# Optimization experiments

Measured on AMD Instinct MI355X. Metric: run time of the kernel, lower is better.

Reference implementation:

```python
import jax, jax.numpy as jnp
import numpy as np

# Model dims (match init_kwargs / Mamba2 defaults)
B, T = 2, 4096
D_MODEL = 1024
D_STATE = 128
D_CONV = 4
EXPAND = 2
D_INNER = EXPAND * D_MODEL          # 2048
HEADDIM = 64                        # Mamba2 default
NHEADS = D_INNER // HEADDIM         # 32
D_IN_PROJ = 2 * D_INNER + 2 * D_STATE + NHEADS  # z, xBC, dt
CONV_DIM = D_INNER + 2 * D_STATE    # conv over x, B, C


def setup_inputs() -> dict:
    key = jax.random.key(0)
    ks = jax.random.split(key, 8)
    return {
        "x": jax.random.normal(ks[0], (B, D_MODEL, T), jnp.float32),
        "ln_w": jnp.ones((D_MODEL,), jnp.float32),
        "ln_b": jnp.zeros((D_MODEL,), jnp.float32),
        "W_in": jax.random.normal(ks[1], (D_IN_PROJ, D_MODEL), jnp.float32) * 0.02,
        "conv_w": jax.random.normal(ks[2], (CONV_DIM, D_CONV), jnp.float32) * 0.2,
        "conv_b": jnp.zeros((CONV_DIM,), jnp.float32),
        "dt_bias": jax.random.normal(ks[3], (NHEADS,), jnp.float32) * 0.5,
        "A_log": jnp.log(0.5 + jax.random.uniform(ks[4], (NHEADS,)) * 4.0),
        "D": jnp.ones((NHEADS,), jnp.float32),
        "rms_w": jnp.ones((D_INNER,), jnp.float32),
        "W_out": jax.random.normal(ks[5], (D_MODEL, D_INNER), jnp.float32) * 0.02,
        "hidden_state": jnp.zeros((B, NHEADS, HEADDIM, D_STATE), jnp.float32),
    }


def _silu(v):
    return v * jax.nn.sigmoid(v)


def _forward(x, ln_w, ln_b, W_in, conv_w, conv_b, dt_bias, A_log, Dp, rms_w, W_out, h0):
    # x: [B, d_model, T] -> [B, T, d_model]
    xt = x.transpose(0, 2, 1)
    # LayerNorm
    mu = xt.mean(-1, keepdims=True)
    var = ((xt - mu) ** 2).mean(-1, keepdims=True)
    xn = (xt - mu) * jax.lax.rsqrt(var + 1e-5) * ln_w + ln_b
    # in_proj -> z, xBC, dt
    zxbcdt = xn @ W_in.T                       # [B, T, D_IN_PROJ]
    z = zxbcdt[..., :D_INNER]
    xBC = zxbcdt[..., D_INNER:D_INNER + CONV_DIM]
    dt = zxbcdt[..., D_INNER + CONV_DIM:]      # [B, T, H]
    # causal depthwise conv over time (kernel D_CONV), then SiLU
    xpad = jnp.pad(xBC, ((0, 0), (D_CONV - 1, 0), (0, 0)))
    conv = sum(conv_w[:, k] * xpad[:, k:k + T, :] for k in range(D_CONV)) + conv_b
    xBC = _silu(conv)
    xin = xBC[..., :D_INNER].reshape(B, T, NHEADS, HEADDIM)
    Bm = xBC[..., D_INNER:D_INNER + D_STATE]   # [B, T, N]
    Cm = xBC[..., D_INNER + D_STATE:]          # [B, T, N]
    # selective SSM parameters
    dt = jax.nn.softplus(dt + dt_bias)         # [B, T, H]
    A = -jnp.exp(A_log)                        # [H]
    dA = jnp.exp(dt * A)                       # [B, T, H]
    xdt = xin * dt[..., None]                  # [B, T, H, P]

    def step(h, inp):
        dA_t, x_t, B_t, C_t = inp              # [B,H], [B,H,P], [B,N], [B,N]
        h = h * dA_t[:, :, None, None] + x_t[..., None] * B_t[:, None, None, :]
        y_t = jnp.einsum("bhpn,bn->bhp", h, C_t)
        return h, y_t

    hT, ys = jax.lax.scan(
        step, h0,
        (dA.transpose(1, 0, 2), xdt.transpose(1, 0, 2, 3),
         Bm.transpose(1, 0, 2), Cm.transpose(1, 0, 2)))
    y = ys.transpose(1, 0, 2, 3) + Dp[None, None, :, None] * xin  # [B,T,H,P]
    y = y.reshape(B, T, D_INNER)
    # gated RMSNorm then out_proj
    g = y * _silu(z)
    g = g * jax.lax.rsqrt((g * g).mean(-1, keepdims=True) + 1e-5) * rms_w
    out = (g @ W_out.T).transpose(0, 2, 1)     # back to [B, d_model, T]
    return out, hT


def reference(x, ln_w, ln_b, W_in, conv_w, conv_b, dt_bias, A_log, D, rms_w, W_out, hidden_state):
    return _forward(x, ln_w, ln_b, W_in, conv_w, conv_b, dt_bias, A_log, D, rms_w, W_out, hidden_state)
```

## Files before the change

kernel.cpp:

```cpp
#include <hip/hip_runtime.h>
#include <hip/hip_bf16.h>
#include <math.h>

#define BB 2
#define TT 4096
#define DM 1024
#define DSTATE 128
#define DI 2048
#define HD 64
#define NH 32
#define DIP 4384
#define CD 2304

#define NC 8
#define CL 512
#define FL 64
#define FPC (CL / FL)
#define SELEMS ((size_t)BB * NH * HD * DSTATE)

#define NP1 4480
#define KSPLIT 16

typedef __attribute__((ext_vector_type(8))) short bf16x8;
typedef __attribute__((ext_vector_type(4))) float f32x4;

__device__ inline void gload16(const void* g, void* l) {
    __builtin_amdgcn_global_load_lds(
        (const __attribute__((address_space(1))) void*)g,
        (__attribute__((address_space(3))) void*)l, 16, 0, 0);
}

__device__ inline short f2bs(float f) {
    __hip_bfloat16 h = __float2bfloat16(f);
    union { __hip_bfloat16 h; short s; } u;
    u.h = h;
    return u.s;
}
__device__ inline float b2f(short s) {
    union { float f; unsigned u; } u;
    u.u = ((unsigned)(unsigned short)s) << 16;
    return u.f;
}

__global__ __launch_bounds__(256) void ln_stats_kernel(const float* __restrict__ x,
                                                       float* __restrict__ mu,
                                                       float* __restrict__ rs) {
    __shared__ float sred[2][8][32];
    int tid = threadIdx.x;
    int tl = tid & 31;
    int ds = tid >> 5;
    int t = (blockIdx.x & 127) * 32 + tl;
    int b = blockIdx.x >> 7;
    const float* xb = x + (size_t)b * DM * TT + (size_t)ds * 128 * TT + t;
    float s = 0.f, ss = 0.f;
#pragma unroll 8
    for (int d = 0; d < 128; d++) {
        float v = xb[(size_t)d * TT];
        s += v;
        ss += v * v;
    }
    sred[0][ds][tl] = s;
    sred[1][ds][tl] = ss;
    __syncthreads();
    if (tid < 32) {
        float st = 0.f, sst = 0.f;
#pragma unroll
        for (int q = 0; q < 8; q++) { st += sred[0][q][tid]; sst += sred[1][q][tid]; }
        float m = st * (1.f / DM);
        float var = sst * (1.f / DM) - m * m;
        int idx = b * TT + (blockIdx.x & 127) * 32 + tid;
        mu[idx] = m;
        rs[idx] = rsqrtf(var + 1e-5f);
    }
}

__global__ __launch_bounds__(256) void xn_kernel(const float* __restrict__ x,
                                                 const float* __restrict__ mu,
                                                 const float* __restrict__ rs,
                                                 const float* __restrict__ ln_w,
                                                 const float* __restrict__ ln_b,
                                                 __hip_bfloat16* __restrict__ xn) {
    __shared__ float tile[64][65];
    int tid = threadIdx.x;
    int t0 = blockIdx.x * 64, d0 = blockIdx.y * 64, b = blockIdx.z;
#pragma unroll
    for (int i = 0; i < 64; i += 4) {
        int dl = i + (tid >> 6);
        tile[dl][tid & 63] = x[(size_t)b * DM * TT + (size_t)(d0 + dl) * TT + t0 + (tid & 63)];
    }
    __syncthreads();
#pragma unroll
    for (int i = 0; i < 64; i += 8) {
        int tl = i + (tid >> 5);
        int kk = (tid & 31) * 2;
        int m = b * TT + t0 + tl;
        float mu_m = mu[m], rs_m = rs[m];
        float v0 = (tile[kk][tl] - mu_m) * rs_m * ln_w[d0 + kk] + ln_b[d0 + kk];
        float v1 = (tile[kk + 1][tl] - mu_m) * rs_m * ln_w[d0 + kk + 1] + ln_b[d0 + kk + 1];
        __hip_bfloat162 pk;
        pk.x = __float2bfloat16(v0);
        pk.y = __float2bfloat16(v1);
        *(__hip_bfloat162*)(xn + (size_t)m * DM + d0 + kk) = pk;
    }
}

__global__ __launch_bounds__(256) void cvt_pad_kernel(const float* __restrict__ src,
                                                      __hip_bfloat16* __restrict__ dst,
                                                      int src_n, int tot_n) {
    int i = (blockIdx.x * 256 + threadIdx.x) * 4;
    if (i >= tot_n) return;
    float4 v = (i < src_n) ? *(const float4*)(src + i) : make_float4(0.f, 0.f, 0.f, 0.f);
    __hip_bfloat162 p0, p1;
    p0.x = __float2bfloat16(v.x); p0.y = __float2bfloat16(v.y);
    p1.x = __float2bfloat16(v.z); p1.y = __float2bfloat16(v.w);
    *(__hip_bfloat162*)(dst + i) = p0;
    *(__hip_bfloat162*)(dst + i + 2) = p1;
}

__global__ __launch_bounds__(256) void gemm1_mfma(const __hip_bfloat16* __restrict__ Wb,
                                                  const __hip_bfloat16* __restrict__ xn,
                                                  short* __restrict__ zx) {
    __shared__ short As[128][64];
    __shared__ short Bs[128][64];
    int tid = threadIdx.x;
    int lane = tid & 63;
    int wave = tid >> 6;
    int wr = wave >> 1, wc = wave & 1;
    int id = blockIdx.x;
    int xcd = id & 7;
    int pos = id >> 3;
    int j0 = (pos >> 3) * 128;
    int m0 = (xcd * 8 + (pos & 7)) * 128;
    int srow = tid >> 3;
    int skc = (((tid & 7) ^ ((tid >> 3) & 7)) * 8);

    f32x4 acc[4][4] = {};

    for (int k0 = 0; k0 < DM; k0 += 64) {
        __syncthreads();
#pragma unroll
        for (int q = 0; q < 4; q++) {
            gload16(Wb + (size_t)(j0 + q * 32 + srow) * DM + k0 + skc,
                    ((short*)As) + q * 2048 + wave * 512);
            gload16(xn + (size_t)(m0 + q * 32 + srow) * DM + k0 + skc,
                    ((short*)Bs) + q * 2048 + wave * 512);
        }
        asm volatile("s_waitcnt vmcnt(0)" ::: "memory");
        __syncthreads();
#pragma unroll
        for (int ks = 0; ks < 2; ks++) {
            int pch = (((ks * 4) + (lane >> 4)) ^ (lane & 7)) * 8;
            bf16x8 af[4], bfr[4];
#pragma unroll
            for (int i = 0; i < 4; i++)
                af[i] = *(const bf16x8*)&As[wr * 64 + i * 16 + (lane & 15)][pch];
#pragma unroll
            for (int n = 0; n < 4; n++)
                bfr[n] = *(const bf16x8*)&Bs[wc * 64 + n * 16 + (lane & 15)][pch];
#pragma unroll
            for (int i = 0; i < 4; i++)
#pragma unroll
                for (int n = 0; n < 4; n++)
                    acc[i][n] = __builtin_amdgcn_mfma_f32_16x16x32_bf16(af[i], bfr[n], acc[i][n], 0, 0, 0);
        }
    }
#pragma unroll
    for (int i = 0; i < 4; i++) {
        int j = j0 + wr * 64 + i * 16 + ((lane >> 4) << 2);
        if (j < DIP) {
#pragma unroll
            for (int n = 0; n < 4; n++) {
                int m = m0 + wc * 64 + n * 16 + (lane & 15);
                short4 s4;
                s4.x = f2bs(acc[i][n][0]); s4.y = f2bs(acc[i][n][1]);
                s4.z = f2bs(acc[i][n][2]); s4.w = f2bs(acc[i][n][3]);
                *(short4*)(zx + (size_t)m * DIP + j) = s4;
            }
        }
    }
}

__global__ __launch_bounds__(256) void gemm1_strip(const float* __restrict__ x,
                                                   const float* __restrict__ mu,
                                                   const float* __restrict__ rs,
                                                   const float* __restrict__ ln_w,
                                                   const float* __restrict__ ln_b,
                                                   const float* __restrict__ Win,
                                                   float* __restrict__ partial) {
    __shared__ float As[16][64];
    __shared__ float Ws[64][17];
    int tid = threadIdx.x;
    int tx = tid & 15;
    int ty = tid >> 4;
    int j0 = 4352;
    int kq = blockIdx.x;
    int m0 = blockIdx.y * 64;
    int b = m0 >> 12;
    int t0 = m0 & 4095;
    const float* Xb = x + (size_t)b * DM * TT + t0;

    int lr = tid >> 4;
    int lc = (tid & 15) * 4;
    int wr = tid >> 2;
    int wc = (tid & 3) * 4;

    float acc[4][4] = {};
    int kbeg = kq * (DM / KSPLIT);
    for (int k0 = kbeg; k0 < kbeg + DM / KSPLIT; k0 += 16) {
        float4 xv = *(const float4*)(Xb + (size_t)(k0 + lr) * TT + lc);
        float4 muv = *(const float4*)(&mu[m0 + lc]);
        float4 rsv = *(const float4*)(&rs[m0 + lc]);
        float lw = ln_w[k0 + lr], lb = ln_b[k0 + lr];
        As[lr][lc]     = (xv.x - muv.x) * rsv.x * lw + lb;
        As[lr][lc + 1] = (xv.y - muv.y) * rsv.y * lw + lb;
        As[lr][lc + 2] = (xv.z - muv.z) * rsv.z * lw + lb;
        As[lr][lc + 3] = (xv.w - muv.w) * rsv.w * lw + lb;

        int j = j0 + wr;
        float4 wv = make_float4(0.f, 0.f, 0.f, 0.f);
        if (j < DIP) wv = *(const float4*)(Win + (size_t)j * DM + k0 + wc);
        Ws[wr][wc] = wv.x; Ws[wr][wc + 1] = wv.y; Ws[wr][wc + 2] = wv.z; Ws[wr][wc + 3] = wv.w;
        __syncthreads();
#pragma unroll
        for (int kk = 0; kk < 16; kk++) {
            float4 a4 = *(const float4*)&As[kk][ty * 4];
            float a[4] = {a4.x, a4.y, a4.z, a4.w};
            float bv[4];
#pragma unroll
            for (int n = 0; n < 4; n++) bv[n] = Ws[tx * 4 + n][kk];
#pragma unroll
            for (int i = 0; i < 4; i++)
#pragma unroll
                for (int n = 0; n < 4; n++)
                    acc[i][n] = fmaf(a[i], bv[n], acc[i][n]);
        }
        __syncthreads();
    }
#pragma unroll
    for (int i = 0; i < 4; i++) {
        int m = m0 + ty * 4 + i;
        int hh = tx * 4;
        if (hh < NH) {
            float4 v = make_float4(acc[i][0], acc[i][1], acc[i][2], acc[i][3]);
            *(float4*)(partial + ((size_t)kq * BB * TT + m) * NH + hh) = v;
        }
    }
}

__global__ __launch_bounds__(256) void dt_reduce_kernel(const float* __restrict__ partial,
                                                        const float* __restrict__ dt_bias,
                                                        float* __restrict__ dtv) {
    int i = blockIdx.x * 256 + threadIdx.x;
    int hh = i & (NH - 1);
    float s = 0.f;
#pragma unroll
    for (int kq = 0; kq < KSPLIT; kq++)
        s += partial[(size_t)kq * BB * TT * NH + i];
    float raw = s + dt_bias[hh];
    dtv[i] = (raw > 20.f) ? raw : log1pf(expf(raw));
}

__global__ __launch_bounds__(256) void conv_kernel(const short* __restrict__ zx,
                                                   const float* __restrict__ cw,
                                                   const float* __restrict__ cb,
                                                   short* __restrict__ xBC) {
    int gid = blockIdx.x * 256 + threadIdx.x;
    int cq = gid % (CD / 8);
    int tq = (gid / (CD / 8)) % (TT / 4);
    int b  = gid / ((CD / 8) * (TT / 4));
    int c = cq * 8, tb = tq * 4;
    const short* src = zx + (size_t)b * TT * DIP + DI + c;

    float wv[8][4];
    float acc[4][8];
#pragma unroll
    for (int e = 0; e < 8; e++) {
        float4 w4 = *(const float4*)(cw + (c + e) * 4);
        wv[e][0] = w4.x; wv[e][1] = w4.y; wv[e][2] = w4.z; wv[e][3] = w4.w;
        float bias = cb[c + e];
#pragma unroll
        for (int o = 0; o < 4; o++) acc[o][e] = bias;
    }

#pragma unroll
    for (int r = 0; r < 7; r++) {
        int ts = tb - 3 + r;
        if (ts >= 0) {
            bf16x8 v = *(const bf16x8*)(src + (size_t)ts * DIP);
            float rowf[8];
#pragma unroll
            for (int e = 0; e < 8; e++) rowf[e] = b2f(v[e]);
#pragma unroll
            for (int o = 0; o < 4; o++) {
                if (o <= r && r <= o + 3) {
                    int k = r - o;
#pragma unroll
                    for (int e = 0; e < 8; e++)
                        acc[o][e] = fmaf(wv[e][k], rowf[e], acc[o][e]);
                }
            }
        }
    }
#pragma unroll
    for (int o = 0; o < 4; o++) {
        short out[8];
#pragma unroll
        for (int e = 0; e < 8; e++) {
            float sg = 1.f / (1.f + expf(-acc[o][e]));
            out[e] = f2bs(acc[o][e] * sg);
        }
        *(bf16x8*)(xBC + ((size_t)b * TT + tb + o) * CD + c) = *(bf16x8*)out;
    }
}

__global__ __launch_bounds__(256, 2) void scan_reduce_ssd(const short* __restrict__ xBC,
                                                          const float* __restrict__ dtg,
                                                          const float* __restrict__ A_log,
                                                          float* __restrict__ S,
                                                          float* __restrict__ P) {
    int tid = threadIdx.x;
    int wave = tid >> 6, lane = tid & 63;
    int l4 = lane >> 4, l16 = lane & 15;
    int c = blockIdx.x, hh = blockIdx.y, b = blockIdx.z;
    int cbase = c * CL;

    __shared__ __align__(16) short BtL[64][136];
    __shared__ __align__(16) short XdL[64][72];
    __shared__ __align__(16) float sdt[64];
    __shared__ __align__(16) float sL[64];
    __shared__ __align__(16) float sW[64];

    f32x4 acc_h[2][4];
#pragma unroll
    for (int i = 0; i < 2; i++)
#pragma unroll
        for (int pq = 0; pq < 4; pq++) acc_h[i][pq] = (f32x4){0.f, 0.f, 0.f, 0.f};
    float Lsum = 0.f;

    float expA = expf(A_log[hh]);
    const float* dtb = dtg + (size_t)b * TT * NH + hh;
    const short* xb = xBC + (size_t)b * TT * CD;

#pragma unroll 1
    for (int f = 0; f < FPC; f++) {
        int t0 = cbase + f * FL;
        if (tid < 64) {
            float val = dtb[(size_t)(t0 + tid) * NH];
            sdt[tid] = val;
            float v = -expA * val;
#pragma unroll
            for (int off = 1; off < 64; off <<= 1) {
                float u = __shfl_up(v, off);
                if (lane >= off) v += u;
            }
            sL[tid] = v;
            float lt = __shfl(v, 63);
            sW[tid] = expf(lt - v);
        }
        {
            int r = tid >> 2, q = tid & 3;
            const short* bs = xb + (size_t)(t0 + r) * CD + DI + q * 32;
#pragma unroll
            for (int j = 0; j < 4; j++)
                *(bf16x8*)&BtL[r][q * 32 + j * 8] = *(const bf16x8*)(bs + j * 8);
        }
        __syncthreads();
        {
            int s = tid & 63, pg2 = tid >> 6;
            const short* xs = xb + (size_t)(t0 + s) * CD + hh * HD + pg2 * 16;
            float dw = sdt[s] * sW[s];
            bf16x8 v0 = *(const bf16x8*)xs;
            bf16x8 v1 = *(const bf16x8*)(xs + 8);
#pragma unroll
            for (int j = 0; j < 8; j++) XdL[pg2 * 16 + j][s] = f2bs(b2f(v0[j]) * dw);
#pragma unroll
            for (int j = 0; j < 8; j++) XdL[pg2 * 16 + 8 + j][s] = f2bs(b2f(v1[j]) * dw);
        }
        __syncthreads();
        float Lft = sL[63];
        float Pf = expf(Lft);
        Lsum += Lft;
#pragma unroll
        for (int i = 0; i < 2; i++)
#pragma unroll
            for (int pq = 0; pq < 4; pq++) acc_h[i][pq] *= Pf;
#pragma unroll
        for (int ks = 0; ks < 2; ks++) {
            bf16x8 af2[2], bfw[4];
#pragma unroll
            for (int i = 0; i < 2; i++) {
                int nrow = wave * 32 + i * 16 + l16;
                short e[8];
#pragma unroll
                for (int j = 0; j < 8; j++)
                    e[j] = BtL[ks * 32 + l4 * 8 + j][nrow];
                af2[i] = *(bf16x8*)e;
            }
#pragma unroll
            for (int pq = 0; pq < 4; pq++)
                bfw[pq] = *(const bf16x8*)&XdL[pq * 16 + l16][ks * 32 + l4 * 8];
#pragma unroll
            for (int i = 0; i < 2; i++)
#pragma unroll
                for (int pq = 0; pq < 4; pq++)
                    acc_h[i][pq] = __builtin_amdgcn_mfma_f32_16x16x32_bf16(af2[i], bfw[pq], acc_h[i][pq], 0, 0, 0);
        }
        __syncthreads();
    }

    float* Sp = S + (size_t)c * SELEMS + ((size_t)(b * NH + hh) * HD) * DSTATE;
#pragma unroll
    for (int i = 0; i < 2; i++)
#pragma unroll
        for (int pq = 0; pq < 4; pq++) {
            int nb = wave * 32 + i * 16 + (l4 << 2);
            int p = pq * 16 + l16;
            *(f32x4*)(Sp + (size_t)p * DSTATE + nb) = acc_h[i][pq];
        }
    if (tid == 0) P[(c * BB + b) * NH + hh] = expf(Lsum);
}

__global__ __launch_bounds__(256) void scan_combine_kernel(const float* __restrict__ h0,
                                                           const float* __restrict__ P,
                                                           float* __restrict__ S,
                                                           float* __restrict__ hT) {
    size_t tid = (size_t)blockIdx.x * 256 + threadIdx.x;
    int hh = (int)((tid >> 13) & 31);
    int b = (int)(tid >> 18);
    float h = h0[tid];
#pragma unroll
    for (int c = 0; c < NC; c++) {
        float s = S[(size_t)c * SELEMS + tid];
        S[(size_t)c * SELEMS + tid] = h;
        h = fmaf(P[(c * BB + b) * NH + hh], h, s);
    }
    hT[tid] = h;
}

__global__ __launch_bounds__(256, 2) void scan_emit_ssd(const short* __restrict__ xBC,
                                                        const float* __restrict__ dtg,
                                                        const float* __restrict__ A_log,
                                                        const float* __restrict__ S,
                                                        const float* __restrict__ Dp,
                                                        short* __restrict__ ybq) {
    int tid = threadIdx.x;
    int wave = tid >> 6, lane = tid & 63;
    int l4 = lane >> 4, l16 = lane & 15;
    int c = blockIdx.x, hh = blockIdx.y, b = blockIdx.z;
    int cbase = c * CL;

    __shared__ __align__(16) short CtL[64][136];
    __shared__ __align__(16) short BtL[64][136];
    __shared__ __align__(16) short hL[64][132];
    __shared__ __align__(16) short XdL[64][72];
    __shared__ __align__(16) short XdwL[64][72];
    __shared__ __align__(16) short ML[64][72];
    __shared__ __align__(16) float sdt[64];
    __shared__ __align__(16) float sL[64];
    __shared__ __align__(16) float sW[64];
    __shared__ __align__(16) float sRdt[64];

    f32x4 acc_h[2][4];
    {
        const float* Sp = S + (size_t)c * SELEMS + ((size_t)(b * NH + hh) * HD) * DSTATE;
#pragma unroll
        for (int i = 0; i < 2; i++)
#pragma unroll
            for (int pq = 0; pq < 4; pq++) {
                int nb = wave * 32 + i * 16 + (l4 << 2);
                int p = pq * 16 + l16;
                acc_h[i][pq] = *(const f32x4*)(Sp + (size_t)p * DSTATE + nb);
            }
    }

    float expA = expf(A_log[hh]);
    float Dh = Dp[hh];
    const float* dtb = dtg + (size_t)b * TT * NH + hh;
    const short* xb = xBC + (size_t)b * TT * CD;
    short* yb = ybq + (size_t)b * TT * DI + hh * HD;

    int tg = wave >> 1;
    int sg = wave & 1;

#pragma unroll 1
    for (int f = 0; f < FPC; f++) {
        int t0 = cbase + f * FL;

        if (tid < 64) {
            float val = dtb[(size_t)(t0 + tid) * NH];
            sdt[tid] = val;
            float v = -expA * val;
#pragma unroll
            for (int off = 1; off < 64; off <<= 1) {
                float u = __shfl_up(v, off);
                if (lane >= off) v += u;
            }
            sL[tid] = v;
            float lt = __shfl(v, 63);
            sW[tid] = expf(lt - v);
            sRdt[tid] = 1.f / val;
        }
        {
            int r = tid >> 2, q = tid & 3;
            const short* cs = xb + (size_t)(t0 + r) * CD + DI + DSTATE + q * 32;
            const short* bs = xb + (size_t)(t0 + r) * CD + DI + q * 32;
#pragma unroll
            for (int j = 0; j < 4; j++) {
                *(bf16x8*)&CtL[r][q * 32 + j * 8] = *(const bf16x8*)(cs + j * 8);
                *(bf16x8*)&BtL[r][q * 32 + j * 8] = *(const bf16x8*)(bs + j * 8);
            }
        }
#pragma unroll
        for (int i = 0; i < 2; i++)
#pragma unroll
            for (int pq = 0; pq < 4; pq++) {
                int nb = wave * 32 + i * 16 + (l4 << 2);
                int p = pq * 16 + l16;
                *(short2*)&hL[p][nb] = make_short2(f2bs(acc_h[i][pq][0]), f2bs(acc_h[i][pq][1]));
                *(short2*)&hL[p][nb + 2] = make_short2(f2bs(acc_h[i][pq][2]), f2bs(acc_h[i][pq][3]));
            }
        __syncthreads();

        {
            int s = tid & 63, pg = tid >> 6;
            const short* xs = xb + (size_t)(t0 + s) * CD + hh * HD + pg * 16;
            float dts = sdt[s];
            float dw = dts * sW[s];
            bf16x8 v0 = *(const bf16x8*)xs;
            bf16x8 v1 = *(const bf16x8*)(xs + 8);
#pragma unroll
            for (int j = 0; j < 8; j++) {
                float xv = b2f(v0[j]);
                XdL[pg * 16 + j][s] = f2bs(xv * dts);
                XdwL[pg * 16 + j][s] = f2bs(xv * dw);
            }
#pragma unroll
            for (int j = 0; j < 8; j++) {
                float xv = b2f(v1[j]);
                XdL[pg * 16 + 8 + j][s] = f2bs(xv * dts);
                XdwL[pg * 16 + 8 + j][s] = f2bs(xv * dw);
            }
        }
        __syncthreads();

        {
            f32x4 g[2][2] = {};
#pragma unroll
            for (int ks = 0; ks < 4; ks++) {
                bf16x8 af[2], bfm[2];
#pragma unroll
                for (int i = 0; i < 2; i++)
                    af[i] = *(const bf16x8*)&CtL[tg * 32 + i * 16 + l16][ks * 32 + l4 * 8];
#pragma unroll
                for (int n = 0; n < 2; n++)
                    bfm[n] = *(const bf16x8*)&BtL[sg * 32 + n * 16 + l16][ks * 32 + l4 * 8];
#pragma unroll
                for (int i = 0; i < 2; i++)
#pragma unroll
                    for (int n = 0; n < 2; n++)
                        g[i][n] = __builtin_amdgcn_mfma_f32_16x16x32_bf16(af[i], bfm[n], g[i][n], 0, 0, 0);
            }
#pragma unroll
            for (int i = 0; i < 2; i++) {
                int tb2 = tg * 32 + i * 16 + (l4 << 2);
                float4 Lt = *(const float4*)&sL[tb2];
                float Ltr[4] = {Lt.x, Lt.y, Lt.z, Lt.w};
#pragma unroll
                for (int n = 0; n < 2; n++) {
                    int sE = sg * 32 + n * 16 + l16;
                    float Ls = sL[sE];
#pragma unroll
                    for (int r2 = 0; r2 < 4; r2++) {
                        float m = (sE <= tb2 + r2) ? g[i][n][r2] * expf(Ltr[r2] - Ls) : 0.f;
                        ML[tb2 + r2][sE] = f2bs(m);
                    }
                }
            }
        }
        __syncthreads();

        {
            f32x4 ay[2][2] = {};
            f32x4 ai[2][2] = {};
#pragma unroll
            for (int ks = 0; ks < 2; ks++) {
                bf16x8 af[2], bfp[2];
#pragma unroll
                for (int i = 0; i < 2; i++)
                    af[i] = *(const bf16x8*)&ML[tg * 32 + i * 16 + l16][ks * 32 + l4 * 8];
#pragma unroll
                for (int n = 0; n < 2; n++)
                    bfp[n] = *(const bf16x8*)&XdL[sg * 32 + n * 16 + l16][ks * 32 + l4 * 8];
#pragma unroll
                for (int i = 0; i < 2; i++)
#pragma unroll
                    for (int n = 0; n < 2; n++)
                        ay[i][n] = __builtin_amdgcn_mfma_f32_16x16x32_bf16(af[i], bfp[n], ay[i][n], 0, 0, 0);
            }
#pragma unroll
            for (int ks = 0; ks < 4; ks++) {
                bf16x8 af[2], bfh[2];
#pragma unroll
                for (int i = 0; i < 2; i++)
                    af[i] = *(const bf16x8*)&CtL[tg * 32 + i * 16 + l16][ks * 32 + l4 * 8];
#pragma unroll
                for (int n = 0; n < 2; n++) {
                    int prow = sg * 32 + n * 16 + l16;
                    int kb = ks * 32 + l4 * 8;
                    union { bf16x8 v; uint2 u2[2]; } hu;
                    hu.u2[0] = *(const uint2*)&hL[prow][kb];
                    hu.u2[1] = *(const uint2*)&hL[prow][kb + 4];
                    bfh[n] = hu.v;
                }
#pragma unroll
                for (int i = 0; i < 2; i++)
#pragma unroll
                    for (int n = 0; n < 2; n++)
                        ai[i][n] = __builtin_amdgcn_mfma_f32_16x16x32_bf16(af[i], bfh[n], ai[i][n], 0, 0, 0);
            }
            float Lft = sL[63];
#pragma unroll
            for (int i = 0; i < 2; i++) {
                int tb2 = tg * 32 + i * 16 + (l4 << 2);
                float4 Lt = *(const float4*)&sL[tb2];
                float4 Rt = *(const float4*)&sRdt[tb2];
                float Ltr[4] = {Lt.x, Lt.y, Lt.z, Lt.w};
                float Rtr[4] = {Rt.x, Rt.y, Rt.z, Rt.w};
#pragma unroll
                for (int n = 0; n < 2; n++) {
                    int p = sg * 32 + n * 16 + l16;
#pragma unroll
                    for (int r2 = 0; r2 < 4; r2++) {
                        float xv = b2f(XdL[p][tb2 + r2]) * Rtr[r2];
                        float yv = ay[i][n][r2] + expf(Ltr[r2]) * ai[i][n][r2] + Dh * xv;
                        yb[(size_t)(t0 + tb2 + r2) * DI + p] = f2bs(yv);
                    }
                }
            }
            float Pf = expf(Lft);
#pragma unroll
            for (int i = 0; i < 2; i++)
#pragma unroll
                for (int pq = 0; pq < 4; pq++)
                    acc_h[i][pq] *= Pf;
#pragma unroll
            for (int ks = 0; ks < 2; ks++) {
                bf16x8 af2[2], bfw[4];
#pragma unroll
                for (int i = 0; i < 2; i++) {
                    int nrow = wave * 32 + i * 16 + l16;
                    short e[8];
#pragma unroll
                    for (int j = 0; j < 8; j++)
                        e[j] = BtL[ks * 32 + l4 * 8 + j][nrow];
                    af2[i] = *(bf16x8*)e;
                }
#pragma unroll
                for (int pq = 0; pq < 4; pq++)
                    bfw[pq] = *(const bf16x8*)&XdwL[pq * 16 + l16][ks * 32 + l4 * 8];
#pragma unroll
                for (int i = 0; i < 2; i++)
#pragma unroll
                    for (int pq = 0; pq < 4; pq++)
                        acc_h[i][pq] = __builtin_amdgcn_mfma_f32_16x16x32_bf16(af2[i], bfw[pq], acc_h[i][pq], 0, 0, 0);
            }
        }
        __syncthreads();
    }
}

__global__ __launch_bounds__(256) void gate_rms_kernel(const short* __restrict__ ybq,
                                                       const short* __restrict__ zx,
                                                       const float* __restrict__ rw,
                                                       __hip_bfloat16* __restrict__ gq) {
    int m = blockIdx.x;
    int tid = threadIdx.x;
    const short* yr = ybq + (size_t)m * DI;
    const short* zr = zx + (size_t)m * DIP;
    int base = tid * 8;
    float gv[8];
    float ss = 0.f;
    bf16x8 yv8 = *(const bf16x8*)(yr + base);
    bf16x8 zv8 = *(const bf16x8*)(zr + base);
#pragma unroll
    for (int i = 0; i < 8; i++) {
        float y = b2f(yv8[i]);
        float z = b2f(zv8[i]);
        float sg = 1.f / (1.f + expf(-z));
        float gg = y * z * sg;
        gv[i] = gg;
        ss += gg * gg;
    }
#pragma unroll
    for (int off = 1; off < 64; off <<= 1) ss += __shfl_xor(ss, off);
    __shared__ float red[4];
    int w = tid >> 6;
    if ((tid & 63) == 0) red[w] = ss;
    __syncthreads();
    float tot = red[0] + red[1] + red[2] + red[3];
    float r = rsqrtf(tot * (1.f / DI) + 1e-5f);
#pragma unroll
    for (int i = 0; i < 8; i += 2) {
        __hip_bfloat162 p;
        p.x = __float2bfloat16(gv[i] * r * rw[base + i]);
        p.y = __float2bfloat16(gv[i + 1] * r * rw[base + i + 1]);
        *(__hip_bfloat162*)(gq + (size_t)m * DI + base + i) = p;
    }
}

__global__ __launch_bounds__(256) void gemm2_mfma(const __hip_bfloat16* __restrict__ gq,
                                                  const __hip_bfloat16* __restrict__ Wob,
                                                  float* __restrict__ out) {
    __shared__ short As[128][64];
    __shared__ short Bs[128][64];
    int tid = threadIdx.x;
    int lane = tid & 63;
    int wave = tid >> 6;
    int wr = wave >> 1, wc = wave & 1;
    int id = blockIdx.x;
    int xcd = id & 7;
    int pos = id >> 3;
    int j0 = (pos >> 3) * 128;
    int m0 = (xcd * 8 + (pos & 7)) * 128;
    int srow = tid >> 3;
    int skc = (((tid & 7) ^ ((tid >> 3) & 7)) * 8);

    f32x4 acc[4][4] = {};

    for (int k0 = 0; k0 < DI; k0 += 64) {
        __syncthreads();
#pragma unroll
        for (int q = 0; q < 4; q++) {
            gload16(gq + (size_t)(m0 + q * 32 + srow) * DI + k0 + skc,
                    ((short*)As) + q * 2048 + wave * 512);
            gload16(Wob + (size_t)(j0 + q * 32 + srow) * DI + k0 + skc,
                    ((short*)Bs) + q * 2048 + wave * 512);
        }
        asm volatile("s_waitcnt vmcnt(0)" ::: "memory");
        __syncthreads();
#pragma unroll
        for (int ks = 0; ks < 2; ks++) {
            int pch = (((ks * 4) + (lane >> 4)) ^ (lane & 7)) * 8;
            bf16x8 af[4], bfr[4];
#pragma unroll
            for (int i = 0; i < 4; i++)
                af[i] = *(const bf16x8*)&As[wr * 64 + i * 16 + (lane & 15)][pch];
#pragma unroll
            for (int n = 0; n < 4; n++)
                bfr[n] = *(const bf16x8*)&Bs[wc * 64 + n * 16 + (lane & 15)][pch];
#pragma unroll
            for (int i = 0; i < 4; i++)
#pragma unroll
                for (int n = 0; n < 4; n++)
                    acc[i][n] = __builtin_amdgcn_mfma_f32_16x16x32_bf16(af[i], bfr[n], acc[i][n], 0, 0, 0);
        }
    }
#pragma unroll
    for (int i = 0; i < 4; i++) {
        int m = m0 + wr * 64 + i * 16 + ((lane >> 4) << 2);
        int b = m >> 12;
        int t = m & 4095;
#pragma unroll
        for (int n = 0; n < 4; n++) {
            int j = j0 + wc * 64 + n * 16 + (lane & 15);
            *(f32x4*)(out + (size_t)b * DM * TT + (size_t)j * TT + t) = acc[i][n];
        }
    }
}

extern "C" void kernel_launch(void* const* d_in, const int* in_sizes, int n_in,
                              void* d_out, int out_size, void* d_ws, size_t ws_size,
                              hipStream_t stream) {
    const float* x       = (const float*)d_in[0];
    const float* ln_w    = (const float*)d_in[1];
    const float* ln_b    = (const float*)d_in[2];
    const float* W_in    = (const float*)d_in[3];
    const float* conv_w  = (const float*)d_in[4];
    const float* conv_b  = (const float*)d_in[5];
    const float* dt_bias = (const float*)d_in[6];
    const float* A_log   = (const float*)d_in[7];
    const float* Dp      = (const float*)d_in[8];
    const float* rms_w   = (const float*)d_in[9];
    const float* W_out   = (const float*)d_in[10];
    const float* h0      = (const float*)d_in[11];

    float* out = (float*)d_out;
    float* hT = out + (size_t)BB * DM * TT;

    char* ws = (char*)d_ws;
    float* mu   = (float*)(ws + 0);
    float* rs   = (float*)(ws + 32768);
    short* zxq  = (short*)(ws + 65536);
    short* xBCq = (short*)(ws + 71892992);
    __hip_bfloat16* gq  = (__hip_bfloat16*)(ws + 71892992);
    __hip_bfloat16* Wob = (__hip_bfloat16*)(ws + 105447424);
    short* ybq  = (short*)(ws + 109641728);
    __hip_bfloat16* Wb  = (__hip_bfloat16*)(ws + 109641728);
    float* dtv  = (float*)(ws + 176750592);
    __hip_bfloat16* xnb = (__hip_bfloat16*)(ws + 177799168);
    float* S    = (float*)(ws + 177799168);
    float* P    = (float*)(ws + 194576384);
    float* dpart = (float*)(ws + 194578432);

    ln_stats_kernel<<<(TT / 32) * BB, 256, 0, stream>>>(x, mu, rs);
    xn_kernel<<<dim3(TT / 64, DM / 64, BB), 256, 0, stream>>>(x, mu, rs, ln_w, ln_b, xnb);
    cvt_pad_kernel<<<(NP1 * DM) / 1024, 256, 0, stream>>>(W_in, Wb, DIP * DM, NP1 * DM);
    gemm1_mfma<<<(NP1 / 128) * ((BB * TT) / 128), 256, 0, stream>>>(Wb, xnb, zxq);
    gemm1_strip<<<dim3(KSPLIT, (BB * TT) / 64), 256, 0, stream>>>(x, mu, rs, ln_w, ln_b, W_in, dpart);
    dt_reduce_kernel<<<(BB * TT * NH) / 256, 256, 0, stream>>>(dpart, dt_bias, dtv);
    conv_kernel<<<(BB * (TT / 4) * (CD / 8)) / 256, 256, 0, stream>>>(zxq, conv_w, conv_b, xBCq);
    scan_reduce_ssd<<<dim3(NC, NH, BB), 256, 0, stream>>>(xBCq, dtv, A_log, S, P);
    scan_combine_kernel<<<(int)(SELEMS / 256), 256, 0, stream>>>(h0, P, S, hT);
    scan_emit_ssd<<<dim3(NC, NH, BB), 256, 0, stream>>>(xBCq, dtv, A_log, S, Dp, ybq);
    cvt_pad_kernel<<<(DM * DI) / 1024, 256, 0, stream>>>(W_out, Wob, DM * DI, DM * DI);
    gate_rms_kernel<<<BB * TT, 256, 0, stream>>>(ybq, zxq, rms_w, gq);
    gemm2_mfma<<<((BB * TT) / 128) * (DM / 128), 256, 0, stream>>>(gq, Wob, out);
}
```

Measured before the change: 318.2 us.

## Double-buffer gemm1 LDS tiles and enlarge block tile to 128x256

Replaces the in_proj MFMA GEMM with a 512-thread version that computes a 128x256 output tile per block. It uses a K step of 32 and double-buffers the shared-memory tiles, so the next slice's global loads are issued before the current slice's MFMAs. The goal is to hide global load latency behind compute and reuse each weight tile across more rows. In exchange there are more K iterations, each still ending with a full vmcnt wait and barrier, and the grid has fewer blocks.

```diff
diff --git a/kernel.cpp b/kernel.cpp
--- a/kernel.cpp
+++ b/kernel.cpp
@@ -117,60 +117,68 @@
     *(__hip_bfloat162*)(dst + i + 2) = p1;
 }
 
-__global__ __launch_bounds__(256) void gemm1_mfma(const __hip_bfloat16* __restrict__ Wb,
-                                                  const __hip_bfloat16* __restrict__ xn,
-                                                  short* __restrict__ zx) {
-    __shared__ short As[128][64];
-    __shared__ short Bs[128][64];
+__global__ __launch_bounds__(512, 4) void gemm1_mfma256(const __hip_bfloat16* __restrict__ Wb,
+                                                        const __hip_bfloat16* __restrict__ xn,
+                                                        short* __restrict__ zx) {
+    __shared__ short As[2][128][32];
+    __shared__ short Bs[2][256][32];
     int tid = threadIdx.x;
     int lane = tid & 63;
     int wave = tid >> 6;
-    int wr = wave >> 1, wc = wave & 1;
+    int wm = wave >> 1;
+    int wn = wave & 1;
     int id = blockIdx.x;
     int xcd = id & 7;
     int pos = id >> 3;
-    int j0 = (pos >> 3) * 128;
-    int m0 = (xcd * 8 + (pos & 7)) * 128;
-    int srow = tid >> 3;
-    int skc = (((tid & 7) ^ ((tid >> 3) & 7)) * 8);
+    int j0 = (pos >> 2) * 128;
+    int m0 = (xcd * 4 + (pos & 3)) * 256;
+    int arow = wave * 16 + (lane >> 2);
+    int skc = (((lane & 3) ^ ((lane >> 2) & 3)) * 8);
 
     f32x4 acc[4][4] = {};
 
-    for (int k0 = 0; k0 < DM; k0 += 64) {
-        __syncthreads();
-#pragma unroll
-        for (int q = 0; q < 4; q++) {
-            gload16(Wb + (size_t)(j0 + q * 32 + srow) * DM + k0 + skc,
-                    ((short*)As) + q * 2048 + wave * 512);
-            gload16(xn + (size_t)(m0 + q * 32 + srow) * DM + k0 + skc,
-                    ((short*)Bs) + q * 2048 + wave * 512);
-        }
+    gload16(Wb + (size_t)(j0 + arow) * DM + skc, ((short*)As) + wave * 512);
+    gload16(xn + (size_t)(m0 + arow) * DM + skc, ((short*)Bs) + wave * 512);
+    gload16(xn + (size_t)(m0 + 128 + arow) * DM + skc, ((short*)Bs) + 4096 + wave * 512);
+    asm volatile("s_waitcnt vmcnt(0)" ::: "memory");
+    __syncthreads();
+
+    int buf = 0;
+    for (int kt = 0; kt < 32; kt++) {
+        if (kt < 31) {
+            int k0 = (kt + 1) * 32;
+            int ob = buf ^ 1;
+            gload16(Wb + (size_t)(j0 + arow) * DM + k0 + skc,
+                    ((short*)As) + ob * 4096 + wave * 512);
+            gload16(xn + (size_t)(m0 + arow) * DM + k0 + skc,
+                    ((short*)Bs) + ob * 8192 + wave * 512);
+            gload16(xn + (size_t)(m0 + 128 + arow) * DM + k0 + skc,
+                    ((short*)Bs) + ob * 8192 + 4096 + wave * 512);
+        }
+        int pch = ((lane >> 4) ^ (lane & 3)) * 8;
+        bf16x8 af[4], bfr[4];
+#pragma unroll
+        for (int i = 0; i < 4; i++)
+            af[i] = *(const bf16x8*)&As[buf][wn * 64 + i * 16 + (lane & 15)][pch];
+#pragma unroll
+        for (int n = 0; n < 4; n++)
+            bfr[n] = *(const bf16x8*)&Bs[buf][wm * 64 + n * 16 + (lane & 15)][pch];
+#pragma unroll
+        for (int i = 0; i < 4; i++)
+#pragma unroll
+            for (int n = 0; n < 4; n++)
+                acc[i][n] = __builtin_amdgcn_mfma_f32_16x16x32_bf16(af[i], bfr[n], acc[i][n], 0, 0, 0);
         asm volatile("s_waitcnt vmcnt(0)" ::: "memory");
         __syncthreads();
-#pragma unroll
-        for (int ks = 0; ks < 2; ks++) {
-            int pch = (((ks * 4) + (lane >> 4)) ^ (lane & 7)) * 8;
-            bf16x8 af[4], bfr[4];
-#pragma unroll
-            for (int i = 0; i < 4; i++)
-                af[i] = *(const bf16x8*)&As[wr * 64 + i * 16 + (lane & 15)][pch];
-#pragma unroll
-            for (int n = 0; n < 4; n++)
-                bfr[n] = *(const bf16x8*)&Bs[wc * 64 + n * 16 + (lane & 15)][pch];
-#pragma unroll
-            for (int i = 0; i < 4; i++)
-#pragma unroll
-                for (int n = 0; n < 4; n++)
-                    acc[i][n] = __builtin_amdgcn_mfma_f32_16x16x32_bf16(af[i], bfr[n], acc[i][n], 0, 0, 0);
-        }
+        buf ^= 1;
     }
 #pragma unroll
     for (int i = 0; i < 4; i++) {
-        int j = j0 + wr * 64 + i * 16 + ((lane >> 4) << 2);
+        int j = j0 + wn * 64 + i * 16 + ((lane >> 4) << 2);
         if (j < DIP) {
 #pragma unroll
             for (int n = 0; n < 4; n++) {
-                int m = m0 + wc * 64 + n * 16 + (lane & 15);
+                int m = m0 + wm * 64 + n * 16 + (lane & 15);
                 short4 s4;
                 s4.x = f2bs(acc[i][n][0]); s4.y = f2bs(acc[i][n][1]);
                 s4.z = f2bs(acc[i][n][2]); s4.w = f2bs(acc[i][n][3]);
@@ -805,7 +813,7 @@
     ln_stats_kernel<<<(TT / 32) * BB, 256, 0, stream>>>(x, mu, rs);
     xn_kernel<<<dim3(TT / 64, DM / 64, BB), 256, 0, stream>>>(x, mu, rs, ln_w, ln_b, xnb);
     cvt_pad_kernel<<<(NP1 * DM) / 1024, 256, 0, stream>>>(W_in, Wb, DIP * DM, NP1 * DM);
-    gemm1_mfma<<<(NP1 / 128) * ((BB * TT) / 128), 256, 0, stream>>>(Wb, xnb, zxq);
+    gemm1_mfma256<<<(NP1 / 128) * ((BB * TT) / 256), 512, 0, stream>>>(Wb, xnb, zxq);
     gemm1_strip<<<dim3(KSPLIT, (BB * TT) / 64), 256, 0, stream>>>(x, mu, rs, ln_w, ln_b, W_in, dpart);
     dt_reduce_kernel<<<(BB * TT * NH) / 256, 256, 0, stream>>>(dpart, dt_bias, dtv);
     conv_kernel<<<(BB * (TT / 4) * (CD / 8)) / 256, 256, 0, stream>>>(zxq, conv_w, conv_b, xBCq);
```

Result: slower. 335.1 us (+5.3%).
